# Kernel tuning notes

Hardware: AMD Instinct MI355X
Metric: run time of the kernel (lower is better)

The kernel has to match this reference:

```python
import jax, jax.numpy as jnp
import numpy as np

BS, NQ, NC = 8, 100, 81      # batch, queries, classes (COCO-like)
M = 160                      # total targets across batch (20 per image)
H = W = 256                  # mask resolution
P = H * W                    # pixels per mask

COST_CLASS = 1.0
COST_MASK = 1.0
COST_DICE = 1.0


def setup_inputs() -> dict:
    key = jax.random.key(0)
    k1, k2, k3, k4 = jax.random.split(key, 4)
    return {
        "pred_logits": jax.random.normal(k1, (BS, NQ, NC), dtype=jnp.float32),
        "pred_masks": jax.random.normal(k2, (BS, NQ, H, W), dtype=jnp.float32),
        "tgt_ids": jax.random.randint(k3, (M,), 0, NC),
        # binary ground-truth masks, flattened to [M, P]
        "tgt_mask": jnp.round(jax.random.uniform(k4, (M, P), dtype=jnp.float32)),
    }


def reference(pred_logits, pred_masks, tgt_ids, tgt_mask):
    bs, nq = pred_logits.shape[:2]
    N = bs * nq

    # ---- classification cost: -softmax(logits)[:, tgt_ids]  -> [N, M]
    out_prob = jax.nn.softmax(pred_logits.reshape(N, -1), axis=-1)
    cost_class = -out_prob[:, tgt_ids]

    x = pred_masks.reshape(N, -1)          # [N, P] mask logits
    t = tgt_mask                           # [M, P] binary targets
    p = x.shape[1]

    # ---- pairwise BCE-with-logits cost, mean over pixels.
    # bce(x, t) = max(x,0) - x*t + log1p(exp(-|x|)); mean_p splits into a
    # per-prediction row term minus a matmul cross term (avoids the N x M x P blowup).
    pos = jnp.maximum(x, 0.0) + jnp.log1p(jnp.exp(-jnp.abs(x)))   # [N, P]
    row = pos.sum(axis=1)                                          # [N]
    cross = x @ t.T                                                # [N, M]
    cost_mask = (row[:, None] - cross) / p

    # ---- pairwise dice cost: 1 - (2<s,t> + 1) / (sum s + sum t + 1)
    s = jax.nn.sigmoid(x)                                          # [N, P]
    numerator = 2.0 * (s @ t.T)                                    # [N, M]
    denominator = s.sum(axis=1)[:, None] + t.sum(axis=1)[None, :]  # [N, M]
    cost_dice = 1.0 - (numerator + 1.0) / (denominator + 1.0)

    C = COST_CLASS * cost_class + COST_MASK * cost_mask + COST_DICE * cost_dice
    return C.reshape(bs, nq, -1)           # [bs, nq, M] cost matrix
```

## Files before the change

kernel.cpp:

```cpp
#include <hip/hip_runtime.h>
#include <cmath>

#define NROWS 800
#define NCLS  81
#define MT    160
#define PPX   65536
#define SSPLIT 32
#define CHUNK 2048
#define BK    128
#define STEPS (CHUNK / BK)
#define RPB   32
#define RB    25

#define OFF_TBF   0
#define SZ_TBF    (MT * PPX)
#define OFF_CROSS (SZ_TBF)
#define OFF_SDOT  (OFF_CROSS + NROWS * MT * 4)
#define OFF_ROW   (OFF_SDOT + NROWS * MT * 4)
#define OFF_SSUM  (OFF_ROW + NROWS * 4)
#define OFF_TSUM  (OFF_SSUM + NROWS * 4)
#define OFF_PROB  (OFF_TSUM + MT * 4)
#define OFF_END   (OFF_PROB + NROWS * NCLS * 4)

typedef __attribute__((ext_vector_type(4))) float f32x4;
typedef long i64;

typedef __attribute__((address_space(3))) char lds_char;
typedef const __attribute__((address_space(1))) char glob_char;

__global__ __launch_bounds__(256) void prep_kernel(const float* __restrict__ tgt_mask,
                                                   char* __restrict__ ws) {
    int g = blockIdx.x * 256 + threadIdx.x;
    int m = g >> 13;
    int kc = g & 8191;
    const float4* src = (const float4*)(tgt_mask + (size_t)m * PPX + (kc << 3));
    float4 a = src[0], b = src[1];
    float part = a.x + a.y + a.z + a.w + b.x + b.y + b.z + b.w;

    unsigned w0 = __builtin_amdgcn_cvt_pk_fp8_f32(a.x, a.y, 0, false);
    w0 = __builtin_amdgcn_cvt_pk_fp8_f32(a.z, a.w, w0, true);
    unsigned w1 = __builtin_amdgcn_cvt_pk_fp8_f32(b.x, b.y, 0, false);
    w1 = __builtin_amdgcn_cvt_pk_fp8_f32(b.z, b.w, w1, true);

    int group = kc >> 4;
    int c = (kc >> 1) & 7;
    int h = kc & 1;
    uint2 o; o.x = w0; o.y = w1;
    *(uint2*)(ws + OFF_TBF + (size_t)m * PPX + (size_t)group * 128
              + (size_t)(c ^ (m & 7)) * 16 + h * 8) = o;

    #pragma unroll
    for (int mk = 32; mk; mk >>= 1) part += __shfl_xor(part, mk);
    __shared__ float wsum[4];
    if ((threadIdx.x & 63) == 0) wsum[threadIdx.x >> 6] = part;
    __syncthreads();
    if (threadIdx.x == 0) {
        float tot = wsum[0] + wsum[1] + wsum[2] + wsum[3];
        atomicAdd((float*)(ws + OFF_TSUM) + m, tot);
    }
}

__global__ __launch_bounds__(64) void softmax_kernel(const float* __restrict__ logits,
                                                     float* __restrict__ prob) {
    int n = blockIdx.x;
    int l = threadIdx.x;
    const float* row = logits + n * NCLS;
    float v0 = row[l];
    float v1 = (l + 64 < NCLS) ? row[l + 64] : -INFINITY;
    float mx = fmaxf(v0, v1);
    #pragma unroll
    for (int mk = 32; mk; mk >>= 1) mx = fmaxf(mx, __shfl_xor(mx, mk));
    float e0 = __expf(v0 - mx);
    float e1 = (l + 64 < NCLS) ? __expf(v1 - mx) : 0.f;
    float s = e0 + e1;
    #pragma unroll
    for (int mk = 32; mk; mk >>= 1) s += __shfl_xor(s, mk);
    float inv = 1.f / s;
    prob[n * NCLS + l] = e0 * inv;
    if (l + 64 < NCLS) prob[n * NCLS + l + 64] = e1 * inv;
}

struct XS4 { float4 a, b, c, d; };

__device__ __forceinline__ void loadx(XS4& x, const float* xrow, int st) {
    const float* p = xrow + st * BK;
    x.a = *(const float4*)(p);
    x.b = *(const float4*)(p + 4);
    x.c = *(const float4*)(p + 8);
    x.d = *(const float4*)(p + 12);
}

__device__ __forceinline__ void ew4(const float4 v, unsigned& wx, unsigned& ws_,
                                    float& slog2, float& sg_acc) {
    float s[4]; float vals[4] = {v.x, v.y, v.z, v.w};
    #pragma unroll
    for (int j = 0; j < 4; ++j) {
        float t = vals[j];
        float vl = fminf(t * 1.44269504089f, 126.f);
        float t2 = __builtin_amdgcn_exp2f(vl);
        float d = 1.f + t2;
        float r = __builtin_amdgcn_rcpf(d);
        s[j] = t2 * r;
        slog2 += __builtin_amdgcn_logf(d);
        sg_acc += s[j];
    }
    wx = __builtin_amdgcn_cvt_pk_fp8_f32(vals[0], vals[1], 0, false);
    wx = __builtin_amdgcn_cvt_pk_fp8_f32(vals[2], vals[3], wx, true);
    ws_ = __builtin_amdgcn_cvt_pk_fp8_f32(s[0], s[1], 0, false);
    ws_ = __builtin_amdgcn_cvt_pk_fp8_f32(s[2], s[3], ws_, true);
}

__global__ __launch_bounds__(256) void main_kernel(const float* __restrict__ pred_masks,
                                                   char* __restrict__ ws) {
    __shared__ __align__(16) char lds_t[MT * BK];
    __shared__ __align__(16) char lds_x[RPB * BK];
    __shared__ __align__(16) char lds_s[RPB * BK];

    const int tid = threadIdx.x;
    const int w = tid >> 6, l = tid & 63;
    const int rb = blockIdx.x >> 5;
    const int s = blockIdx.x & 31;
    const int k_base = s * CHUNK;

    const int row = tid >> 3;
    const int c8 = tid & 7;
    const int n_glob = rb * RPB + row;
    const float* xrow = pred_masks + (size_t)n_glob * PPX + k_base + c8 * 16;
    char* xw = lds_x + row * 128 + ((c8 ^ (row & 7)) * 16);
    char* swp = lds_s + row * 128 + ((c8 ^ (row & 7)) * 16);

    const char* tbase = ws + OFF_TBF;

    auto stage_t = [&](int st) {
        const size_t k0 = k_base + st * BK;
        #pragma unroll
        for (int i = 0; i < 5; ++i) {
            int rows_base = w * 40 + i * 8;
            const char* g = tbase + (size_t)(rows_base + (l >> 3)) * PPX
                          + k0 + (size_t)(l & 7) * 16;
            __builtin_amdgcn_global_load_lds((glob_char*)g,
                                             (lds_char*)(lds_t + rows_base * 128),
                                             16, 0, 0);
        }
    };

    const int wr = w & 1, wc = w >> 1;
    const int lrow = l & 15;
    const int inner8 = ((l >> 4) & 1) * 8;
    const int cpair = (l >> 4) >> 1;
    f32x4 accX[5], accS[5];
    #pragma unroll
    for (int i = 0; i < 5; ++i) { accX[i] = (f32x4)(0.f); accS[i] = (f32x4)(0.f); }
    float slog2 = 0.f, rs_sg = 0.f;

    XS4 XA, XB;
    loadx(XA, xrow, 0);
    loadx(XB, xrow, 1);

    #pragma unroll 1
    for (int it = 0; it < STEPS; it += 2) {
        #pragma unroll
        for (int half = 0; half < 2; ++half) {
            const int h = it + half;
            stage_t(h);
            __builtin_amdgcn_sched_barrier(0);

            uint4 vx, vs;
            if (half == 0) {
                ew4(XA.a, vx.x, vs.x, slog2, rs_sg);
                ew4(XA.b, vx.y, vs.y, slog2, rs_sg);
                ew4(XA.c, vx.z, vs.z, slog2, rs_sg);
                ew4(XA.d, vx.w, vs.w, slog2, rs_sg);
            } else {
                ew4(XB.a, vx.x, vs.x, slog2, rs_sg);
                ew4(XB.b, vx.y, vs.y, slog2, rs_sg);
                ew4(XB.c, vx.z, vs.z, slog2, rs_sg);
                ew4(XB.d, vx.w, vs.w, slog2, rs_sg);
            }
            *(uint4*)xw = vx;
            *(uint4*)swp = vs;

            int tr = h + 2; if (tr >= STEPS) tr = STEPS - 1;
            if (half == 0) loadx(XA, xrow, tr);
            else           loadx(XB, xrow, tr);

            __builtin_amdgcn_sched_barrier(0);
            asm volatile("s_waitcnt vmcnt(4) lgkmcnt(0)" ::: "memory");
            __builtin_amdgcn_sched_barrier(0);
            __builtin_amdgcn_s_barrier();
            __builtin_amdgcn_sched_barrier(0);

            #pragma unroll
            for (int ks = 0; ks < 4; ++ks) {
                const int arow = wr * 16 + lrow;
                const int ac = (2 * ks + cpair) ^ (arow & 7);
                i64 ax = *(const i64*)(lds_x + arow * 128 + ac * 16 + inner8);
                i64 as_ = *(const i64*)(lds_s + arow * 128 + ac * 16 + inner8);
                #pragma unroll
                for (int cf = 0; cf < 5; ++cf) {
                    const int mrow = (wc * 5 + cf) * 16 + lrow;
                    const int bc = (2 * ks + cpair) ^ (mrow & 7);
                    i64 bv = *(const i64*)(lds_t + mrow * 128 + bc * 16 + inner8);
                    accX[cf] = __builtin_amdgcn_mfma_f32_16x16x32_fp8_fp8(ax, bv, accX[cf], 0, 0, 0);
                    accS[cf] = __builtin_amdgcn_mfma_f32_16x16x32_fp8_fp8(as_, bv, accS[cf], 0, 0, 0);
                }
            }

            asm volatile("s_waitcnt lgkmcnt(0)" ::: "memory");
            __builtin_amdgcn_sched_barrier(0);
            __builtin_amdgcn_s_barrier();
            __builtin_amdgcn_sched_barrier(0);
        }
    }

    asm volatile("s_waitcnt vmcnt(0)" ::: "memory");

    float rs_sp = slog2 * 0.69314718056f;
    rs_sp += __shfl_xor(rs_sp, 1); rs_sp += __shfl_xor(rs_sp, 2); rs_sp += __shfl_xor(rs_sp, 4);
    rs_sg += __shfl_xor(rs_sg, 1); rs_sg += __shfl_xor(rs_sg, 2); rs_sg += __shfl_xor(rs_sg, 4);
    float* acc_row = (float*)(ws + OFF_ROW);
    float* acc_ssum = (float*)(ws + OFF_SSUM);
    if ((tid & 7) == 0) {
        atomicAdd(acc_row + n_glob, rs_sp);
        atomicAdd(acc_ssum + n_glob, rs_sg);
    }

    float* acc_cross = (float*)(ws + OFF_CROSS);
    float* acc_sdot = (float*)(ws + OFF_SDOT);
    #pragma unroll
    for (int cf = 0; cf < 5; ++cf) {
        int mcol = (wc * 5 + cf) * 16 + lrow;
        #pragma unroll
        for (int i = 0; i < 4; ++i) {
            int nrow = rb * RPB + wr * 16 + (l >> 4) * 4 + i;
            atomicAdd(acc_cross + nrow * MT + mcol, accX[cf][i]);
            atomicAdd(acc_sdot + nrow * MT + mcol, accS[cf][i]);
        }
    }
}

__global__ __launch_bounds__(256) void final_kernel(const int* __restrict__ tgt_ids,
                                                    const char* __restrict__ ws,
                                                    float* __restrict__ out) {
    int idx = blockIdx.x * 256 + threadIdx.x;
    int n = idx / MT;
    int m = idx - n * MT;
    const float* prob = (const float*)(ws + OFF_PROB);
    const float* acc_cross = (const float*)(ws + OFF_CROSS);
    const float* acc_sdot = (const float*)(ws + OFF_SDOT);
    const float* acc_row = (const float*)(ws + OFF_ROW);
    const float* acc_ssum = (const float*)(ws + OFF_SSUM);
    const float* tsum = (const float*)(ws + OFF_TSUM);

    float cls = -prob[n * NCLS + tgt_ids[m]];
    float cmask = (acc_row[n] - acc_cross[idx]) * (1.f / PPX);
    float cdice = 1.f - (2.f * acc_sdot[idx] + 1.f) / (acc_ssum[n] + tsum[m] + 1.f);
    out[idx] = cls + cmask + cdice;
}

extern "C" void kernel_launch(void* const* d_in, const int* in_sizes, int n_in,
                              void* d_out, int out_size, void* d_ws, size_t ws_size,
                              hipStream_t stream) {
    const float* pred_logits = (const float*)d_in[0];
    const float* pred_masks  = (const float*)d_in[1];
    const int*   tgt_ids     = (const int*)d_in[2];
    const float* tgt_mask    = (const float*)d_in[3];
    char* ws = (char*)d_ws;

    (void)hipMemsetAsync(ws + OFF_CROSS, 0, OFF_END - OFF_CROSS, stream);
    prep_kernel<<<5120, 256, 0, stream>>>(tgt_mask, ws);
    softmax_kernel<<<NROWS, 64, 0, stream>>>(pred_logits, (float*)(ws + OFF_PROB));
    main_kernel<<<RB * SSPLIT, 256, 0, stream>>>(pred_masks, ws);
    final_kernel<<<500, 256, 0, stream>>>(tgt_ids, ws, (float*)d_out);
}
```

Before: 117.1 us.

## Double-buffer LDS tiles to overlap next-step staging with MFMA compute

Doubles the LDS buffers for the target, x and sigmoid tiles. Step h+1 is staged and its elementwise work done while step h's MFMAs run, which cuts the two barriers per step down to one. A prologue primes buffer 0 and the x-register prefetch moves one step further ahead. This doubles LDS use per block, which may lower occupancy, and it relies on the vmcnt wait counts being correct to avoid races.

```diff
diff --git a/kernel.cpp b/kernel.cpp
--- a/kernel.cpp
+++ b/kernel.cpp
@@ -112,9 +112,9 @@
 
 __global__ __launch_bounds__(256) void main_kernel(const float* __restrict__ pred_masks,
                                                    char* __restrict__ ws) {
-    __shared__ __align__(16) char lds_t[MT * BK];
-    __shared__ __align__(16) char lds_x[RPB * BK];
-    __shared__ __align__(16) char lds_s[RPB * BK];
+    __shared__ __align__(16) char lds_t[2][MT * BK];
+    __shared__ __align__(16) char lds_x[2][RPB * BK];
+    __shared__ __align__(16) char lds_s[2][RPB * BK];
 
     const int tid = threadIdx.x;
     const int w = tid >> 6, l = tid & 63;
@@ -126,12 +126,11 @@
     const int c8 = tid & 7;
     const int n_glob = rb * RPB + row;
     const float* xrow = pred_masks + (size_t)n_glob * PPX + k_base + c8 * 16;
-    char* xw = lds_x + row * 128 + ((c8 ^ (row & 7)) * 16);
-    char* swp = lds_s + row * 128 + ((c8 ^ (row & 7)) * 16);
+    const int xoff = row * 128 + ((c8 ^ (row & 7)) * 16);
 
     const char* tbase = ws + OFF_TBF;
 
-    auto stage_t = [&](int st) {
+    auto stage_t = [&](int buf, int st) {
         const size_t k0 = k_base + st * BK;
         #pragma unroll
         for (int i = 0; i < 5; ++i) {
@@ -139,7 +138,7 @@
             const char* g = tbase + (size_t)(rows_base + (l >> 3)) * PPX
                           + k0 + (size_t)(l & 7) * 16;
             __builtin_amdgcn_global_load_lds((glob_char*)g,
-                                             (lds_char*)(lds_t + rows_base * 128),
+                                             (lds_char*)(lds_t[buf] + rows_base * 128),
                                              16, 0, 0);
         }
     };
@@ -154,62 +153,77 @@
     float slog2 = 0.f, rs_sg = 0.f;
 
     XS4 XA, XB;
+
+    stage_t(0, 0);
+    __builtin_amdgcn_sched_barrier(0);
     loadx(XA, xrow, 0);
     loadx(XB, xrow, 1);
+    {
+        uint4 vx, vs;
+        ew4(XA.a, vx.x, vs.x, slog2, rs_sg);
+        ew4(XA.b, vx.y, vs.y, slog2, rs_sg);
+        ew4(XA.c, vx.z, vs.z, slog2, rs_sg);
+        ew4(XA.d, vx.w, vs.w, slog2, rs_sg);
+        *(uint4*)(lds_x[0] + xoff) = vx;
+        *(uint4*)(lds_s[0] + xoff) = vs;
+    }
+    loadx(XA, xrow, 2);
+    __builtin_amdgcn_sched_barrier(0);
+    asm volatile("s_waitcnt vmcnt(8) lgkmcnt(0)" ::: "memory");
+    __builtin_amdgcn_sched_barrier(0);
+    __builtin_amdgcn_s_barrier();
+    __builtin_amdgcn_sched_barrier(0);
 
     #pragma unroll 1
     for (int it = 0; it < STEPS; it += 2) {
         #pragma unroll
         for (int half = 0; half < 2; ++half) {
             const int h = it + half;
-            stage_t(h);
-            __builtin_amdgcn_sched_barrier(0);
-
-            uint4 vx, vs;
-            if (half == 0) {
-                ew4(XA.a, vx.x, vs.x, slog2, rs_sg);
-                ew4(XA.b, vx.y, vs.y, slog2, rs_sg);
-                ew4(XA.c, vx.z, vs.z, slog2, rs_sg);
-                ew4(XA.d, vx.w, vs.w, slog2, rs_sg);
-            } else {
-                ew4(XB.a, vx.x, vs.x, slog2, rs_sg);
-                ew4(XB.b, vx.y, vs.y, slog2, rs_sg);
-                ew4(XB.c, vx.z, vs.z, slog2, rs_sg);
-                ew4(XB.d, vx.w, vs.w, slog2, rs_sg);
+            if (h + 1 < STEPS) {
+                stage_t(half ^ 1, h + 1);
+                __builtin_amdgcn_sched_barrier(0);
+                uint4 vx, vs;
+                if (half == 0) {
+                    ew4(XB.a, vx.x, vs.x, slog2, rs_sg);
+                    ew4(XB.b, vx.y, vs.y, slog2, rs_sg);
+                    ew4(XB.c, vx.z, vs.z, slog2, rs_sg);
+                    ew4(XB.d, vx.w, vs.w, slog2, rs_sg);
+                } else {
+                    ew4(XA.a, vx.x, vs.x, slog2, rs_sg);
+                    ew4(XA.b, vx.y, vs.y, slog2, rs_sg);
+                    ew4(XA.c, vx.z, vs.z, slog2, rs_sg);
+                    ew4(XA.d, vx.w, vs.w, slog2, rs_sg);
+                }
+                *(uint4*)(lds_x[half ^ 1] + xoff) = vx;
+                *(uint4*)(lds_s[half ^ 1] + xoff) = vs;
+                int tr = h + 3; if (tr >= STEPS) tr = STEPS - 1;
+                if (half == 0) loadx(XB, xrow, tr);
+                else           loadx(XA, xrow, tr);
+                __builtin_amdgcn_sched_barrier(0);
             }
-            *(uint4*)xw = vx;
-            *(uint4*)swp = vs;
-
-            int tr = h + 2; if (tr >= STEPS) tr = STEPS - 1;
-            if (half == 0) loadx(XA, xrow, tr);
-            else           loadx(XB, xrow, tr);
-
-            __builtin_amdgcn_sched_barrier(0);
-            asm volatile("s_waitcnt vmcnt(4) lgkmcnt(0)" ::: "memory");
-            __builtin_amdgcn_sched_barrier(0);
-            __builtin_amdgcn_s_barrier();
-            __builtin_amdgcn_sched_barrier(0);
 
             #pragma unroll
             for (int ks = 0; ks < 4; ++ks) {
                 const int arow = wr * 16 + lrow;
                 const int ac = (2 * ks + cpair) ^ (arow & 7);
-                i64 ax = *(const i64*)(lds_x + arow * 128 + ac * 16 + inner8);
-                i64 as_ = *(const i64*)(lds_s + arow * 128 + ac * 16 + inner8);
+                i64 ax = *(const i64*)(lds_x[half] + arow * 128 + ac * 16 + inner8);
+                i64 as_ = *(const i64*)(lds_s[half] + arow * 128 + ac * 16 + inner8);
                 #pragma unroll
                 for (int cf = 0; cf < 5; ++cf) {
                     const int mrow = (wc * 5 + cf) * 16 + lrow;
                     const int bc = (2 * ks + cpair) ^ (mrow & 7);
-                    i64 bv = *(const i64*)(lds_t + mrow * 128 + bc * 16 + inner8);
+                    i64 bv = *(const i64*)(lds_t[half] + mrow * 128 + bc * 16 + inner8);
                     accX[cf] = __builtin_amdgcn_mfma_f32_16x16x32_fp8_fp8(ax, bv, accX[cf], 0, 0, 0);
                     accS[cf] = __builtin_amdgcn_mfma_f32_16x16x32_fp8_fp8(as_, bv, accS[cf], 0, 0, 0);
                 }
             }
 
-            asm volatile("s_waitcnt lgkmcnt(0)" ::: "memory");
-            __builtin_amdgcn_sched_barrier(0);
-            __builtin_amdgcn_s_barrier();
-            __builtin_amdgcn_sched_barrier(0);
+            if (h + 1 < STEPS) {
+                asm volatile("s_waitcnt vmcnt(4) lgkmcnt(0)" ::: "memory");
+                __builtin_amdgcn_sched_barrier(0);
+                __builtin_amdgcn_s_barrier();
+                __builtin_amdgcn_sched_barrier(0);
+            }
         }
     }
 
```

After: 113.6 us, median of 2. -3.0%, faster.

## Double-buffer target tile in LDS to prefetch next step during MFMA

Applied to the files above, without the earlier changes.

Makes the LDS target tile double-buffered. The load for step h+1 is issued before step h's elementwise and MFMA work, so the global-to-LDS transfer overlaps compute instead of being waited on each step. The wait/barrier placement is reorganized around the new schedule, and the clamp before exp2 in the sigmoid/softplus path is dropped. This doubles the target-tile LDS footprint, which may reduce occupancy. Without the clamp, large logits can give inf, which risks NaN or inf in the per-pixel terms.

```diff
diff --git a/kernel.cpp b/kernel.cpp
--- a/kernel.cpp
+++ b/kernel.cpp
@@ -96,8 +96,7 @@
     #pragma unroll
     for (int j = 0; j < 4; ++j) {
         float t = vals[j];
-        float vl = fminf(t * 1.44269504089f, 126.f);
-        float t2 = __builtin_amdgcn_exp2f(vl);
+        float t2 = __builtin_amdgcn_exp2f(t * 1.44269504089f);
         float d = 1.f + t2;
         float r = __builtin_amdgcn_rcpf(d);
         s[j] = t2 * r;
@@ -112,7 +111,7 @@
 
 __global__ __launch_bounds__(256) void main_kernel(const float* __restrict__ pred_masks,
                                                    char* __restrict__ ws) {
-    __shared__ __align__(16) char lds_t[MT * BK];
+    __shared__ __align__(16) char lds_t[2][MT * BK];
     __shared__ __align__(16) char lds_x[RPB * BK];
     __shared__ __align__(16) char lds_s[RPB * BK];
 
@@ -126,12 +125,11 @@
     const int c8 = tid & 7;
     const int n_glob = rb * RPB + row;
     const float* xrow = pred_masks + (size_t)n_glob * PPX + k_base + c8 * 16;
-    char* xw = lds_x + row * 128 + ((c8 ^ (row & 7)) * 16);
-    char* swp = lds_s + row * 128 + ((c8 ^ (row & 7)) * 16);
+    const int xoff = row * 128 + ((c8 ^ (row & 7)) * 16);
 
     const char* tbase = ws + OFF_TBF;
 
-    auto stage_t = [&](int st) {
+    auto stage_t = [&](int buf, int st) {
         const size_t k0 = k_base + st * BK;
         #pragma unroll
         for (int i = 0; i < 5; ++i) {
@@ -139,7 +137,7 @@
             const char* g = tbase + (size_t)(rows_base + (l >> 3)) * PPX
                           + k0 + (size_t)(l & 7) * 16;
             __builtin_amdgcn_global_load_lds((glob_char*)g,
-                                             (lds_char*)(lds_t + rows_base * 128),
+                                             (lds_char*)(lds_t[buf] + rows_base * 128),
                                              16, 0, 0);
         }
     };
@@ -154,16 +152,26 @@
     float slog2 = 0.f, rs_sg = 0.f;
 
     XS4 XA, XB;
+
+    stage_t(0, 0);
+    __builtin_amdgcn_sched_barrier(0);
     loadx(XA, xrow, 0);
     loadx(XB, xrow, 1);
+    __builtin_amdgcn_sched_barrier(0);
+    asm volatile("s_waitcnt vmcnt(8)" ::: "memory");
+    __builtin_amdgcn_sched_barrier(0);
+    __builtin_amdgcn_s_barrier();
+    __builtin_amdgcn_sched_barrier(0);
 
     #pragma unroll 1
     for (int it = 0; it < STEPS; it += 2) {
         #pragma unroll
         for (int half = 0; half < 2; ++half) {
             const int h = it + half;
-            stage_t(h);
-            __builtin_amdgcn_sched_barrier(0);
+            if (h + 1 < STEPS) {
+                stage_t(half ^ 1, h + 1);
+                __builtin_amdgcn_sched_barrier(0);
+            }
 
             uint4 vx, vs;
             if (half == 0) {
@@ -177,15 +185,15 @@
                 ew4(XB.c, vx.z, vs.z, slog2, rs_sg);
                 ew4(XB.d, vx.w, vs.w, slog2, rs_sg);
             }
-            *(uint4*)xw = vx;
-            *(uint4*)swp = vs;
+            *(uint4*)(lds_x + xoff) = vx;
+            *(uint4*)(lds_s + xoff) = vs;
 
             int tr = h + 2; if (tr >= STEPS) tr = STEPS - 1;
             if (half == 0) loadx(XA, xrow, tr);
             else           loadx(XB, xrow, tr);
-
             __builtin_amdgcn_sched_barrier(0);
-            asm volatile("s_waitcnt vmcnt(4) lgkmcnt(0)" ::: "memory");
+
+            asm volatile("s_waitcnt lgkmcnt(0)" ::: "memory");
             __builtin_amdgcn_sched_barrier(0);
             __builtin_amdgcn_s_barrier();
             __builtin_amdgcn_sched_barrier(0);
@@ -200,16 +208,18 @@
                 for (int cf = 0; cf < 5; ++cf) {
                     const int mrow = (wc * 5 + cf) * 16 + lrow;
                     const int bc = (2 * ks + cpair) ^ (mrow & 7);
-                    i64 bv = *(const i64*)(lds_t + mrow * 128 + bc * 16 + inner8);
+                    i64 bv = *(const i64*)(lds_t[half] + mrow * 128 + bc * 16 + inner8);
                     accX[cf] = __builtin_amdgcn_mfma_f32_16x16x32_fp8_fp8(ax, bv, accX[cf], 0, 0, 0);
                     accS[cf] = __builtin_amdgcn_mfma_f32_16x16x32_fp8_fp8(as_, bv, accS[cf], 0, 0, 0);
                 }
             }
 
-            asm volatile("s_waitcnt lgkmcnt(0)" ::: "memory");
-            __builtin_amdgcn_sched_barrier(0);
-            __builtin_amdgcn_s_barrier();
-            __builtin_amdgcn_sched_barrier(0);
+            if (h + 1 < STEPS) {
+                asm volatile("s_waitcnt vmcnt(4) lgkmcnt(0)" ::: "memory");
+                __builtin_amdgcn_sched_barrier(0);
+                __builtin_amdgcn_s_barrier();
+                __builtin_amdgcn_sched_barrier(0);
+            }
         }
     }
 
```

Measured after the change: 116.3 us. About the same (-0.7%).
